# Performance work log

Hardware: AMD Instinct MI355X
Metric: run time of the kernel (lower is better)

## Reference

```python
import jax, jax.numpy as jnp
import numpy as np
from jax import lax

B, C = 16, 1024          # batch, in_channels (= spectral length)
N_HEAD = 8
N_FEAT = 512
CH = N_FEAT // N_HEAD    # 64 per-head channels
EPS = 1e-5


def setup_inputs() -> dict:
    key = jax.random.key(0)
    ks = jax.random.split(key, 9)
    x = jax.random.normal(ks[0], (B, C), dtype=jnp.float32)
    # BatchNorm1d (inference mode) params / running stats
    bn_gamma = jax.random.normal(ks[1], (C,), dtype=jnp.float32) * 0.1 + 1.0
    bn_beta = jax.random.normal(ks[2], (C,), dtype=jnp.float32) * 0.1
    bn_mean = jax.random.normal(ks[3], (C,), dtype=jnp.float32) * 0.1
    bn_var = jax.random.uniform(ks[4], (C,), dtype=jnp.float32, minval=0.5, maxval=1.5)
    # in_conv: Conv1d(1, 3*N_FEAT, kernel=3, stride=1, pad=1) -> weight [O, I, K]
    w_in = jax.random.normal(ks[5], (3 * N_FEAT, 1, 3), dtype=jnp.float32) * (1.0 / np.sqrt(3))
    b_in = jax.random.normal(ks[6], (3 * N_FEAT,), dtype=jnp.float32) * 0.02
    # proj_h: Conv1d(N_FEAT, 1, kernel=1). zero_module zeros it at init; use
    # nonzero values so the reference exercises the full graph (trained state).
    w_out = jax.random.normal(ks[7], (1, N_FEAT, 1), dtype=jnp.float32) * (1.0 / np.sqrt(N_FEAT))
    b_out = jax.random.normal(ks[8], (1,), dtype=jnp.float32) * 0.02
    return {"x": x, "bn_gamma": bn_gamma, "bn_beta": bn_beta, "bn_mean": bn_mean,
            "bn_var": bn_var, "w_in": w_in, "b_in": b_in, "w_out": w_out, "b_out": b_out}


def reference(x, bn_gamma, bn_beta, bn_mean, bn_var, w_in, b_in, w_out, b_out):
    b, c = x.shape
    # BatchNorm1d on [b, c] input (eval mode, per-channel stats)
    xn = (x - bn_mean) * jax.lax.rsqrt(bn_var + EPS) * bn_gamma + bn_beta
    x1 = xn[:, None, :]  # [b, 1, c]
    # Conv1d(1 -> 3*N_FEAT, k=3, pad=1)
    qkv = lax.conv_general_dilated(
        x1, w_in, window_strides=(1,), padding=((1, 1),),
        dimension_numbers=("NCH", "OIH", "NCH")) + b_in[None, :, None]  # [b, 3F, c]
    # QKVAttentionLegacy: reshape to [b*H, 3*ch, c], split, scaled dot-product
    qkv = qkv.reshape(b * N_HEAD, 3 * CH, c)
    q, k, v = jnp.split(qkv, 3, axis=1)          # each [b*H, ch, c]
    scale = CH ** -0.25
    w = jnp.einsum("bct,bcs->bts", q * scale, k * scale)  # [b*H, c, c]
    w = jax.nn.softmax(w, axis=-1)
    a = jnp.einsum("bts,bcs->bct", w, v)          # [b*H, ch, c]
    h = a.reshape(b, N_FEAT, c)
    # proj_h: 1x1 conv N_FEAT -> 1
    h = jnp.einsum("of,bft->bot", w_out[:, :, 0][None].squeeze(0)[None].squeeze(0)[None] if False else w_out[:, :, 0], h) + b_out[None, :, None]  # [b, 1, c]
    return (h + x1).reshape(b, c)
```

## Files before the change

### kernel.cpp

```cpp
#include <hip/hip_runtime.h>
#include <math.h>

#define NB 16
#define SEQ 1024
#define NHEAD 8

typedef __attribute__((ext_vector_type(4))) float f32x4;

__global__ void __launch_bounds__(256) k_fused(
    const float* __restrict__ x, const float* __restrict__ gam,
    const float* __restrict__ be, const float* __restrict__ mu,
    const float* __restrict__ va, const float* __restrict__ w_in,
    const float* __restrict__ b_in, const float* __restrict__ w_out,
    const float* __restrict__ b_out, float* __restrict__ out) {
  __shared__ float xsl[1032];
  __shared__ float vps[NHEAD][1032];
  __shared__ float Ms[NHEAD][16];
  __shared__ float hcs[NHEAD][4];
  __shared__ float rsum[NHEAD][32];

  int bid = blockIdx.x;
  int b = bid >> 5, chunk = bid & 31;
  int tid = threadIdx.x;

  int t4 = tid * 4;
  f32x4 xv  = *(const f32x4*)(x + b*SEQ + t4);
  f32x4 muv = *(const f32x4*)(mu + t4);
  f32x4 vav = *(const f32x4*)(va + t4);
  f32x4 gv  = *(const f32x4*)(gam + t4);
  f32x4 bev = *(const f32x4*)(be + t4);
  f32x4 xn4;
  #pragma unroll
  for (int u = 0; u < 4; ++u)
    xn4[u] = (xv[u] - muv[u]) * rsqrtf(vav[u] + 1e-5f) * gv[u] + bev[u];
  *(f32x4*)(xsl + t4) = xn4;
  if (tid < 8) xsl[1024 + tid] = 0.f;

  const float QS2 = 0.125f * 1.4426950408889634f;
  if (tid < 128) {
    int hh = tid >> 4, ij = tid & 15, i = ij >> 2, j = ij & 3;
    int oq = hh * 192, ok = oq + 64;
    float acc = 0.f;
    #pragma unroll 8
    for (int c = 0; c < 64; ++c) {
      float wq = (i < 3) ? w_in[(oq + c)*3 + i] : b_in[oq + c];
      float wk = (j < 3) ? w_in[(ok + c)*3 + j] : b_in[ok + c];
      acc = fmaf(wq, wk, acc);
    }
    Ms[hh][ij] = acc * QS2;
  } else if (tid < 160) {
    int idx = tid - 128, hh = idx >> 2, jj = idx & 3;
    int ov = hh * 192 + 128;
    float acc = 0.f;
    #pragma unroll 8
    for (int c = 0; c < 64; ++c) {
      float wv = (jj < 3) ? w_in[(ov + c)*3 + jj] : b_in[ov + c];
      acc = fmaf(w_out[hh*64 + c], wv, acc);
    }
    hcs[hh][jj] = acc;
  }
  __syncthreads();

  int h = tid >> 5, tl = tid & 31;
  {
    float hc0 = hcs[h][0], hc1 = hcs[h][1], hc2 = hcs[h][2], hc3 = hcs[h][3];
    #pragma unroll 4
    for (int k2 = 0; k2 < 32; ++k2) {
      int s = k2*32 + tl;
      float xm = (s > 0) ? xsl[s-1] : 0.f;
      vps[h][s] = fmaf(hc0, xm, fmaf(hc1, xsl[s], fmaf(hc2, xsl[s+1], hc3)));
    }
    if (tl < 8) vps[h][1024 + tl] = 0.f;
  }
  __syncthreads();

  int t = chunk*32 + tl;
  float um = (t > 0) ? xsl[t-1] : 0.f;
  float u0 = xsl[t], up = xsl[t+1];
  const float* Mh = Ms[h];
  float a0 = fmaf(um, Mh[0], fmaf(u0, Mh[4],  fmaf(up, Mh[8],  Mh[12])));
  float a1 = fmaf(um, Mh[1], fmaf(u0, Mh[5],  fmaf(up, Mh[9],  Mh[13])));
  float a2 = fmaf(um, Mh[2], fmaf(u0, Mh[6],  fmaf(up, Mh[10], Mh[14])));
  float a3 = fmaf(um, Mh[3], fmaf(u0, Mh[7],  fmaf(up, Mh[11], Mh[15])));

  const f32x4* x4 = (const f32x4*)xsl;
  const f32x4* v4 = (const f32x4*)&vps[h][0];
  float ss = 0.f, dd = 0.f;
  f32x4 cA = x4[0], vA = v4[0];
  f32x4 cB = x4[1], vB = v4[1];
  float prevW = 0.f;

#define STEP(XM, X0, XP, VV) { \
  float sc = fmaf(a0, (XM), fmaf(a1, (X0), fmaf(a2, (XP), a3))); \
  float p = __builtin_amdgcn_exp2f(sc); \
  ss += p; dd = fmaf(p, (VV), dd); }

  #pragma unroll 4
  for (int k = 0; k < 256; ++k) {
    f32x4 cC = x4[k+2];
    f32x4 vC = v4[k+2];
    STEP(prevW, cA.x, cA.y, vA.x)
    STEP(cA.x,  cA.y, cA.z, vA.y)
    STEP(cA.y,  cA.z, cA.w, vA.z)
    STEP(cA.z,  cA.w, cB.x, vA.w)
    prevW = cA.w; cA = cB; cB = cC; vA = vB; vB = vC;
  }
#undef STEP

  rsum[h][tl] = dd / ss;
  __syncthreads();

  if (tid < 32) {
    int to = chunk*32 + tid;
    float acc = xsl[to] + b_out[0];
    #pragma unroll
    for (int hh = 0; hh < NHEAD; ++hh) acc += rsum[hh][tid];
    out[b*SEQ + to] = acc;
  }
}

extern "C" void kernel_launch(void* const* d_in, const int* in_sizes, int n_in,
                              void* d_out, int out_size, void* d_ws, size_t ws_size,
                              hipStream_t stream) {
  const float* x   = (const float*)d_in[0];
  const float* g   = (const float*)d_in[1];
  const float* be  = (const float*)d_in[2];
  const float* mu  = (const float*)d_in[3];
  const float* va  = (const float*)d_in[4];
  const float* win = (const float*)d_in[5];
  const float* bin = (const float*)d_in[6];
  const float* wo  = (const float*)d_in[7];
  const float* bo  = (const float*)d_in[8];
  float* out = (float*)d_out;
  (void)d_ws; (void)ws_size; (void)in_sizes; (void)n_in; (void)out_size;

  hipLaunchKernelGGL(k_fused, dim3(NB * 32), dim3(256), 0, stream,
                     x, g, be, mu, va, win, bin, wo, bo, out);
}
```

Before: 102.7 us.

## Split key loop across four thread groups with 1024-thread blocks

Each block now uses 1024 threads, with four groups each processing a quarter of the key positions for every head/query pair. Partial softmax denominators and weighted sums are stored in shared memory and combined before the head reduction. This is meant to raise occupancy and shorten the serial exp/accumulate loop per thread. It adds a shared-memory reduction step and an extra barrier, and uses scalar loads for the normalization.

```diff
diff --git a/kernel.cpp b/kernel.cpp
--- a/kernel.cpp
+++ b/kernel.cpp
@@ -7,7 +7,7 @@
 
 typedef __attribute__((ext_vector_type(4))) float f32x4;
 
-__global__ void __launch_bounds__(256) k_fused(
+__global__ void __launch_bounds__(1024) k_fused(
     const float* __restrict__ x, const float* __restrict__ gam,
     const float* __restrict__ be, const float* __restrict__ mu,
     const float* __restrict__ va, const float* __restrict__ w_in,
@@ -17,23 +17,18 @@
   __shared__ float vps[NHEAD][1032];
   __shared__ float Ms[NHEAD][16];
   __shared__ float hcs[NHEAD][4];
+  __shared__ float ssp[4][NHEAD][32];
+  __shared__ float ddp[4][NHEAD][32];
   __shared__ float rsum[NHEAD][32];
 
   int bid = blockIdx.x;
   int b = bid >> 5, chunk = bid & 31;
   int tid = threadIdx.x;
 
-  int t4 = tid * 4;
-  f32x4 xv  = *(const f32x4*)(x + b*SEQ + t4);
-  f32x4 muv = *(const f32x4*)(mu + t4);
-  f32x4 vav = *(const f32x4*)(va + t4);
-  f32x4 gv  = *(const f32x4*)(gam + t4);
-  f32x4 bev = *(const f32x4*)(be + t4);
-  f32x4 xn4;
-  #pragma unroll
-  for (int u = 0; u < 4; ++u)
-    xn4[u] = (xv[u] - muv[u]) * rsqrtf(vav[u] + 1e-5f) * gv[u] + bev[u];
-  *(f32x4*)(xsl + t4) = xn4;
+  {
+    float xv = x[b*SEQ + tid];
+    xsl[tid] = (xv - mu[tid]) * rsqrtf(va[tid] + 1e-5f) * gam[tid] + be[tid];
+  }
   if (tid < 8) xsl[1024 + tid] = 0.f;
 
   const float QS2 = 0.125f * 1.4426950408889634f;
@@ -61,19 +56,20 @@
   }
   __syncthreads();
 
-  int h = tid >> 5, tl = tid & 31;
   {
-    float hc0 = hcs[h][0], hc1 = hcs[h][1], hc2 = hcs[h][2], hc3 = hcs[h][3];
-    #pragma unroll 4
-    for (int k2 = 0; k2 < 32; ++k2) {
-      int s = k2*32 + tl;
+    int hh = tid >> 7, sl = tid & 127;
+    float hc0 = hcs[hh][0], hc1 = hcs[hh][1], hc2 = hcs[hh][2], hc3 = hcs[hh][3];
+    #pragma unroll
+    for (int k2 = 0; k2 < 8; ++k2) {
+      int s = k2*128 + sl;
       float xm = (s > 0) ? xsl[s-1] : 0.f;
-      vps[h][s] = fmaf(hc0, xm, fmaf(hc1, xsl[s], fmaf(hc2, xsl[s+1], hc3)));
+      vps[hh][s] = fmaf(hc0, xm, fmaf(hc1, xsl[s], fmaf(hc2, xsl[s+1], hc3)));
     }
-    if (tl < 8) vps[h][1024 + tl] = 0.f;
+    if (sl < 8) vps[hh][1024 + sl] = 0.f;
   }
   __syncthreads();
 
+  int q = tid >> 8, h = (tid >> 5) & 7, tl = tid & 31;
   int t = chunk*32 + tl;
   float um = (t > 0) ? xsl[t-1] : 0.f;
   float u0 = xsl[t], up = xsl[t+1];
@@ -85,10 +81,11 @@
 
   const f32x4* x4 = (const f32x4*)xsl;
   const f32x4* v4 = (const f32x4*)&vps[h][0];
+  int j0 = q * 64;
   float ss = 0.f, dd = 0.f;
-  f32x4 cA = x4[0], vA = v4[0];
-  f32x4 cB = x4[1], vB = v4[1];
-  float prevW = 0.f;
+  f32x4 cA = x4[j0], vA = v4[j0];
+  f32x4 cB = x4[j0+1], vB = v4[j0+1];
+  float prevW = (q == 0) ? 0.f : xsl[q*256 - 1];
 
 #define STEP(XM, X0, XP, VV) { \
   float sc = fmaf(a0, (XM), fmaf(a1, (X0), fmaf(a2, (XP), a3))); \
@@ -96,9 +93,9 @@
   ss += p; dd = fmaf(p, (VV), dd); }
 
   #pragma unroll 4
-  for (int k = 0; k < 256; ++k) {
-    f32x4 cC = x4[k+2];
-    f32x4 vC = v4[k+2];
+  for (int k = 0; k < 64; ++k) {
+    f32x4 cC = x4[j0 + k + 2];
+    f32x4 vC = v4[j0 + k + 2];
     STEP(prevW, cA.x, cA.y, vA.x)
     STEP(cA.x,  cA.y, cA.z, vA.y)
     STEP(cA.y,  cA.z, cA.w, vA.z)
@@ -107,9 +104,16 @@
   }
 #undef STEP
 
-  rsum[h][tl] = dd / ss;
+  ssp[q][h][tl] = ss;
+  ddp[q][h][tl] = dd;
   __syncthreads();
 
+  if (tid < 256) {
+    float sT = ssp[0][h][tl] + ssp[1][h][tl] + ssp[2][h][tl] + ssp[3][h][tl];
+    float dT = ddp[0][h][tl] + ddp[1][h][tl] + ddp[2][h][tl] + ddp[3][h][tl];
+    rsum[h][tl] = dT / sT;
+  }
+  __syncthreads();
   if (tid < 32) {
     int to = chunk*32 + tid;
     float acc = xsl[to] + b_out[0];
@@ -134,6 +138,6 @@
   float* out = (float*)d_out;
   (void)d_ws; (void)ws_size; (void)in_sizes; (void)n_in; (void)out_size;
 
-  hipLaunchKernelGGL(k_fused, dim3(NB * 32), dim3(256), 0, stream,
+  hipLaunchKernelGGL(k_fused, dim3(NB * 32), dim3(1024), 0, stream,
                      x, g, be, mu, va, win, bin, wo, bo, out);
 }
```

Result: faster. 98.91 us (-3.7%).
